# Optimization experiments

Measured on AMD Instinct MI355X. Metric: run time of the kernel, lower is better.

Reference implementation:

```python
import jax, jax.numpy as jnp
import numpy as np

N_BATCHES = 32
N_LABELS = 100


def setup_inputs() -> dict:
    key = jax.random.key(0)
    ks = jax.random.split(key, 7)
    N, D, P = 16384, 2048, 256
    x = jax.random.normal(ks[0], (N, D), dtype=jnp.float32)
    label = jax.random.randint(ks[1], (N,), 0, N_LABELS, dtype=jnp.int64)
    label_batch = jnp.sort(jax.random.randint(ks[2], (N,), 0, N_BATCHES, dtype=jnp.int64))
    W1_w = jax.random.normal(ks[3], (P, D), dtype=jnp.float32) * 0.02
    W1_b = jax.random.normal(ks[4], (P,), dtype=jnp.float32) * 0.02
    W2_w = jax.random.normal(ks[5], (P, D), dtype=jnp.float32) * 0.02
    W2_b = jax.random.normal(ks[6], (P,), dtype=jnp.float32) * 0.02
    return {"x": x, "label": label, "label_batch": label_batch,
            "W1_w": W1_w, "W1_b": W1_b, "W2_w": W2_w, "W2_b": W2_b}


def _loo_diff_label_mean(x, label, label_batch):
    # For each sample i: mean of x over {j : label_batch[j]==label_batch[i] and label[j]!=label[i]}.
    # Rows with no such j are zero (torch code's `continue`). x is detached in the original.
    N = x.shape[0]
    xs = jax.lax.stop_gradient(x)
    seg = label_batch * N_LABELS + label                      # combined (group,label) key
    n_seg = N_BATCHES * N_LABELS
    ones = jnp.ones((N,), dtype=x.dtype)
    sum_bl = jax.ops.segment_sum(xs, seg, num_segments=n_seg)            # [n_seg, D]
    cnt_bl = jax.ops.segment_sum(ones, seg, num_segments=n_seg)          # [n_seg]
    sum_b = jax.ops.segment_sum(xs, label_batch, num_segments=N_BATCHES)  # [NB, D]
    cnt_b = jax.ops.segment_sum(ones, label_batch, num_segments=N_BATCHES)
    diff_sum = sum_b[label_batch] - sum_bl[seg]               # [N, D]
    diff_cnt = cnt_b[label_batch] - cnt_bl[seg]               # [N]
    safe = jnp.maximum(diff_cnt, 1.0)
    mean = diff_sum / safe[:, None]
    return jnp.where((diff_cnt > 0)[:, None], mean, jnp.zeros_like(mean))


def reference(x, label, label_batch, W1_w, W1_b, W2_w, W2_b):
    calc_mean = _loo_diff_label_mean(x, label, label_batch)   # detached aggregate
    return x @ W1_w.T + W1_b + calc_mean @ W2_w.T + W2_b      # W1(x) + W2(mean)
```

## Files before the change

kernel.cpp:

```cpp
#include <hip/hip_runtime.h>
#include <cstdint>

#define N_SAMPLES 16384
#define DIM 2048
#define PDIM 256
#define NB 32
#define NL 100
#define NSEG (NB * NL)

typedef float floatx4 __attribute__((ext_vector_type(4)));
typedef __bf16 bf16x8 __attribute__((ext_vector_type(8)));

__device__ __forceinline__ unsigned short f32_to_bf16(float f) {
    unsigned int u = __float_as_uint(f);
    u += 0x7fffu + ((u >> 16) & 1u);
    return (unsigned short)(u >> 16);
}
__device__ __forceinline__ unsigned int pack_bf16x2(float a, float b) {
    return (unsigned int)f32_to_bf16(a) | ((unsigned int)f32_to_bf16(b) << 16);
}

__global__ __launch_bounds__(256) void prep_kernel(
    const float* __restrict__ W1w, const float* __restrict__ W1b,
    const float* __restrict__ W2w, const float* __restrict__ W2b,
    const int* __restrict__ label, const int* __restrict__ lbatch,
    unsigned short* __restrict__ Wbf, float* __restrict__ bias,
    int* __restrict__ seg, int* __restrict__ cnt, float* __restrict__ SW2)
{
    int i = blockIdx.x * 256 + threadIdx.x;
    Wbf[i]              = f32_to_bf16(W1w[i]);
    Wbf[PDIM * DIM + i] = f32_to_bf16(W2w[i]);
    if (i < PDIM) bias[i] = W1b[i] + W2b[i];
    if (i < N_SAMPLES) seg[i] = lbatch[i] * NL + label[i];
    if (i < NSEG) cnt[i] = 0;
    if (i < NSEG * PDIM / 2) ((float2*)SW2)[i] = make_float2(0.f, 0.f);
}

__global__ __launch_bounds__(256) void hist_kernel(
    const int* __restrict__ seg, int* __restrict__ cnt)
{
    int i = blockIdx.x * 256 + threadIdx.x;
    atomicAdd(&cnt[seg[i]], 1);
}

__global__ __launch_bounds__(256) void xconv_kernel(
    const float* __restrict__ x, unsigned short* __restrict__ xb)
{
    const size_t idx = (size_t)blockIdx.x * 256 + threadIdx.x;
    const float4 a0 = *(const float4*)(x + idx * 8);
    const float4 a1 = *(const float4*)(x + idx * 8 + 4);
    uint4 o;
    o.x = pack_bf16x2(a0.x, a0.y);
    o.y = pack_bf16x2(a0.z, a0.w);
    o.z = pack_bf16x2(a1.x, a1.y);
    o.w = pack_bf16x2(a1.z, a1.w);
    *(uint4*)(xb + idx * 8) = o;
}

__global__ __launch_bounds__(256) void gemm512_kernel(
    const unsigned short* __restrict__ A,
    const unsigned short* __restrict__ Wbf,
    const float* __restrict__ bias, const int* __restrict__ seg,
    float* __restrict__ out, float* __restrict__ SW2)
{
    constexpr int BM = 128, BN = 128, BK = 32;
    __shared__ __align__(16) unsigned short ldsA[BM * BK];
    __shared__ __align__(16) unsigned short ldsB[BN * BK];
    const int tid = threadIdx.x;
    const int lane = tid & 63;
    const int wave = tid >> 6;
    const int wr = wave >> 1, wc = wave & 1;
    const int quad = lane >> 4, l15 = lane & 15;
    const int m0 = blockIdx.x * BM;
    const int n0 = blockIdx.y * BN;
    const int srow = lane >> 2, schunk = lane & 3;

    floatx4 acc[4][4];
    #pragma unroll
    for (int i = 0; i < 4; ++i)
        #pragma unroll
        for (int j = 0; j < 4; ++j) acc[i][j] = (floatx4){0.f, 0.f, 0.f, 0.f};

    const unsigned short* Abase = A + (size_t)(m0 + srow) * DIM + schunk * 8;
    const unsigned short* Bbase = Wbf + (size_t)(n0 + srow) * DIM + schunk * 8;

    for (int kk = 0; kk < DIM; kk += BK) {
        __syncthreads();
        #pragma unroll
        for (int ch = wave; ch < BM / 16; ch += 4)
            __builtin_amdgcn_global_load_lds(
                (const __attribute__((address_space(1))) void*)(Abase + (size_t)ch * 16 * DIM + kk),
                (__attribute__((address_space(3))) void*)&ldsA[ch * 16 * BK], 16, 0, 0);
        #pragma unroll
        for (int ch = wave; ch < BN / 16; ch += 4)
            __builtin_amdgcn_global_load_lds(
                (const __attribute__((address_space(1))) void*)(Bbase + (size_t)ch * 16 * DIM + kk),
                (__attribute__((address_space(3))) void*)&ldsB[ch * 16 * BK], 16, 0, 0);
        __syncthreads();

        bf16x8 af[4], bf[4];
        #pragma unroll
        for (int mi = 0; mi < 4; ++mi)
            af[mi] = *(const bf16x8*)&ldsA[(wr * 64 + mi * 16 + l15) * BK + quad * 8];
        #pragma unroll
        for (int ni = 0; ni < 4; ++ni)
            bf[ni] = *(const bf16x8*)&ldsB[(wc * 64 + ni * 16 + l15) * BK + quad * 8];
        #pragma unroll
        for (int mi = 0; mi < 4; ++mi)
            #pragma unroll
            for (int ni = 0; ni < 4; ++ni)
                acc[mi][ni] = __builtin_amdgcn_mfma_f32_16x16x32_bf16(
                    af[mi], bf[ni], acc[mi][ni], 0, 0, 0);
    }

    if (n0 < PDIM) {
        #pragma unroll
        for (int mi = 0; mi < 4; ++mi) {
            const int rbase = m0 + wr * 64 + mi * 16 + quad * 4;
            #pragma unroll
            for (int ni = 0; ni < 4; ++ni) {
                const int col = n0 + wc * 64 + ni * 16 + l15;
                const float bs = bias[col];
                #pragma unroll
                for (int r = 0; r < 4; ++r)
                    out[(size_t)(rbase + r) * PDIM + col] = acc[mi][ni][r] + bs;
            }
        }
    } else {
        const int c0 = n0 - PDIM;
        #pragma unroll
        for (int mi = 0; mi < 4; ++mi) {
            const int rbase = m0 + wr * 64 + mi * 16 + quad * 4;
            #pragma unroll
            for (int r = 0; r < 4; ++r) {
                const int sr = seg[rbase + r];
                #pragma unroll
                for (int ni = 0; ni < 4; ++ni) {
                    const int col = c0 + wc * 64 + ni * 16 + l15;
                    atomicAdd(&SW2[(size_t)sr * PDIM + col], acc[mi][ni][r]);
                }
            }
        }
    }
}

__global__ __launch_bounds__(256) void finalize_kernel(
    float* __restrict__ SW2, const int* __restrict__ cnt)
{
    const int b = blockIdx.x;
    const int col = threadIdx.x;
    int cb = 0;
    #pragma unroll 4
    for (int l = 0; l < NL; ++l) cb += cnt[b * NL + l];
    float tot = 0.f;
    #pragma unroll 4
    for (int l = 0; l < NL; ++l)
        tot += SW2[(size_t)(b * NL + l) * PDIM + col];
    for (int l = 0; l < NL; ++l) {
        const int s = b * NL + l;
        const int dc = cb - cnt[s];
        const float v = SW2[(size_t)s * PDIM + col];
        SW2[(size_t)s * PDIM + col] = (dc > 0) ? (tot - v) / (float)dc : 0.f;
    }
}

__global__ __launch_bounds__(256) void epilogue_kernel(
    float* __restrict__ out, const float* __restrict__ SW2,
    const int* __restrict__ seg)
{
    const int idx = blockIdx.x * 256 + threadIdx.x;
    const int row = idx >> 6;
    const int c = (idx & 63) * 4;
    float4 v = ((const float4*)out)[idx];
    const float4 s4 = *(const float4*)&SW2[(size_t)seg[row] * PDIM + c];
    v.x += s4.x; v.y += s4.y; v.z += s4.z; v.w += s4.w;
    ((float4*)out)[idx] = v;
}

extern "C" void kernel_launch(void* const* d_in, const int* in_sizes, int n_in,
                              void* d_out, int out_size, void* d_ws, size_t ws_size,
                              hipStream_t stream)
{
    const float* x      = (const float*)d_in[0];
    const int*   label  = (const int*)d_in[1];
    const int*   lbatch = (const int*)d_in[2];
    const float* W1w    = (const float*)d_in[3];
    const float* W1b    = (const float*)d_in[4];
    const float* W2w    = (const float*)d_in[5];
    const float* W2b    = (const float*)d_in[6];
    float* out = (float*)d_out;

    char* ws = (char*)d_ws;
    size_t off = 0;
    auto alloc = [&](size_t bytes) {
        void* p = ws + off;
        off = (off + bytes + 255) & ~(size_t)255;
        return p;
    };
    unsigned short* xb  = (unsigned short*)alloc((size_t)N_SAMPLES * DIM * 2);
    unsigned short* Wbf = (unsigned short*)alloc((size_t)2 * PDIM * DIM * 2);
    float* SW2  = (float*)alloc((size_t)NSEG * PDIM * 4);
    float* bias = (float*)alloc(PDIM * 4);
    int*   seg  = (int*)alloc(N_SAMPLES * 4);
    int*   cnt  = (int*)alloc(NSEG * 4);

    prep_kernel<<<PDIM * DIM / 256, 256, 0, stream>>>(
        W1w, W1b, W2w, W2b, label, lbatch, Wbf, bias, seg, cnt, SW2);

    hist_kernel<<<N_SAMPLES / 256, 256, 0, stream>>>(seg, cnt);

    xconv_kernel<<<(size_t)N_SAMPLES * DIM / 8 / 256, 256, 0, stream>>>(x, xb);

    gemm512_kernel<<<dim3(N_SAMPLES / 128, 4), 256, 0, stream>>>(
        xb, Wbf, bias, seg, out, SW2);

    finalize_kernel<<<NB, 256, 0, stream>>>(SW2, cnt);

    epilogue_kernel<<<(size_t)N_SAMPLES * PDIM / 4 / 256, 256, 0, stream>>>(
        out, SW2, seg);
}
```

Baseline: 305.2 us.

## Split GEMM K dimension in two with atomic accumulation and XCD-aware block mapping

The fused GEMM grid goes from 512 to 1024 blocks by splitting the K dimension into two halves. Partial results are accumulated into the output with atomics, so the output is zeroed in the prep kernel and the bias add moves to the epilogue. Block IDs are remapped so that consecutive blocks on each XCD share M-tiles, which should improve L2 reuse. The aim is better occupancy across the CUs, at the cost of doubled atomic traffic on both the output and the segment sums.

```diff
diff --git a/kernel.cpp b/kernel.cpp
--- a/kernel.cpp
+++ b/kernel.cpp
@@ -25,7 +25,8 @@
     const float* __restrict__ W2w, const float* __restrict__ W2b,
     const int* __restrict__ label, const int* __restrict__ lbatch,
     unsigned short* __restrict__ Wbf, float* __restrict__ bias,
-    int* __restrict__ seg, int* __restrict__ cnt, float* __restrict__ SW2)
+    int* __restrict__ seg, int* __restrict__ cnt, float* __restrict__ SW2,
+    float* __restrict__ out)
 {
     int i = blockIdx.x * 256 + threadIdx.x;
     Wbf[i]              = f32_to_bf16(W1w[i]);
@@ -34,6 +35,9 @@
     if (i < N_SAMPLES) seg[i] = lbatch[i] * NL + label[i];
     if (i < NSEG) cnt[i] = 0;
     if (i < NSEG * PDIM / 2) ((float2*)SW2)[i] = make_float2(0.f, 0.f);
+    const float4 z4 = make_float4(0.f, 0.f, 0.f, 0.f);
+    ((float4*)out)[2 * i]     = z4;
+    ((float4*)out)[2 * i + 1] = z4;
 }
 
 __global__ __launch_bounds__(256) void hist_kernel(
@@ -60,10 +64,10 @@
 __global__ __launch_bounds__(256) void gemm512_kernel(
     const unsigned short* __restrict__ A,
     const unsigned short* __restrict__ Wbf,
-    const float* __restrict__ bias, const int* __restrict__ seg,
+    const int* __restrict__ seg,
     float* __restrict__ out, float* __restrict__ SW2)
 {
-    constexpr int BM = 128, BN = 128, BK = 32;
+    constexpr int BM = 128, BN = 128, BK = 32, KS = 2;
     __shared__ __align__(16) unsigned short ldsA[BM * BK];
     __shared__ __align__(16) unsigned short ldsB[BN * BK];
     const int tid = threadIdx.x;
@@ -71,20 +75,27 @@
     const int wave = tid >> 6;
     const int wr = wave >> 1, wc = wave & 1;
     const int quad = lane >> 4, l15 = lane & 15;
-    const int m0 = blockIdx.x * BM;
-    const int n0 = blockIdx.y * BN;
+
+    const int bid = blockIdx.x;
+    const int j = bid & 7;
+    const int idx = bid >> 3;
+    const int m0 = (j * 16 + (idx & 15)) * BM;
+    const int nz = idx >> 4;
+    const int n0 = (nz & 3) * BN;
+    const int z  = nz >> 2;
+    const int k0 = z * (DIM / KS);
     const int srow = lane >> 2, schunk = lane & 3;
 
     floatx4 acc[4][4];
     #pragma unroll
     for (int i = 0; i < 4; ++i)
         #pragma unroll
-        for (int j = 0; j < 4; ++j) acc[i][j] = (floatx4){0.f, 0.f, 0.f, 0.f};
+        for (int jj = 0; jj < 4; ++jj) acc[i][jj] = (floatx4){0.f, 0.f, 0.f, 0.f};
 
     const unsigned short* Abase = A + (size_t)(m0 + srow) * DIM + schunk * 8;
     const unsigned short* Bbase = Wbf + (size_t)(n0 + srow) * DIM + schunk * 8;
 
-    for (int kk = 0; kk < DIM; kk += BK) {
+    for (int kk = k0; kk < k0 + DIM / KS; kk += BK) {
         __syncthreads();
         #pragma unroll
         for (int ch = wave; ch < BM / 16; ch += 4)
@@ -120,10 +131,9 @@
             #pragma unroll
             for (int ni = 0; ni < 4; ++ni) {
                 const int col = n0 + wc * 64 + ni * 16 + l15;
-                const float bs = bias[col];
                 #pragma unroll
                 for (int r = 0; r < 4; ++r)
-                    out[(size_t)(rbase + r) * PDIM + col] = acc[mi][ni][r] + bs;
+                    atomicAdd(&out[(size_t)(rbase + r) * PDIM + col], acc[mi][ni][r]);
             }
         }
     } else {
@@ -166,14 +176,16 @@
 
 __global__ __launch_bounds__(256) void epilogue_kernel(
     float* __restrict__ out, const float* __restrict__ SW2,
-    const int* __restrict__ seg)
+    const float* __restrict__ bias, const int* __restrict__ seg)
 {
     const int idx = blockIdx.x * 256 + threadIdx.x;
     const int row = idx >> 6;
     const int c = (idx & 63) * 4;
     float4 v = ((const float4*)out)[idx];
+    const float4 b4 = *(const float4*)&bias[c];
     const float4 s4 = *(const float4*)&SW2[(size_t)seg[row] * PDIM + c];
-    v.x += s4.x; v.y += s4.y; v.z += s4.z; v.w += s4.w;
+    v.x += b4.x + s4.x; v.y += b4.y + s4.y;
+    v.z += b4.z + s4.z; v.w += b4.w + s4.w;
     ((float4*)out)[idx] = v;
 }
 
@@ -205,17 +217,16 @@
     int*   cnt  = (int*)alloc(NSEG * 4);
 
     prep_kernel<<<PDIM * DIM / 256, 256, 0, stream>>>(
-        W1w, W1b, W2w, W2b, label, lbatch, Wbf, bias, seg, cnt, SW2);
+        W1w, W1b, W2w, W2b, label, lbatch, Wbf, bias, seg, cnt, SW2, out);
 
     hist_kernel<<<N_SAMPLES / 256, 256, 0, stream>>>(seg, cnt);
 
     xconv_kernel<<<(size_t)N_SAMPLES * DIM / 8 / 256, 256, 0, stream>>>(x, xb);
 
-    gemm512_kernel<<<dim3(N_SAMPLES / 128, 4), 256, 0, stream>>>(
-        xb, Wbf, bias, seg, out, SW2);
+    gemm512_kernel<<<1024, 256, 0, stream>>>(xb, Wbf, seg, out, SW2);
 
     finalize_kernel<<<NB, 256, 0, stream>>>(SW2, cnt);
 
     epilogue_kernel<<<(size_t)N_SAMPLES * PDIM / 4 / 256, 256, 0, stream>>>(
-        out, SW2, seg);
-}
+        out, SW2, bias, seg);
+}
```

New measurement: 343.0 us. +12.4%, slower.

## Fuse fp32-to-bf16 conversion of x into the GEMM's LDS load path

Applied to the files above, without the earlier changes.

Drops the separate x conversion kernel and its bf16 staging buffer. The GEMM now loads fp32 x tiles straight into LDS with an XOR-swizzled layout and converts to bf16 when building the MFMA operands. This removes one full write and read of the converted x. In exchange the GEMM reads twice as many bytes of A per tile (x is read once per N-tile, four times in total), uses more LDS, and does conversion work inside the inner loop.

```diff
diff --git a/kernel.cpp b/kernel.cpp
--- a/kernel.cpp
+++ b/kernel.cpp
@@ -15,9 +15,6 @@
     unsigned int u = __float_as_uint(f);
     u += 0x7fffu + ((u >> 16) & 1u);
     return (unsigned short)(u >> 16);
-}
-__device__ __forceinline__ unsigned int pack_bf16x2(float a, float b) {
-    return (unsigned int)f32_to_bf16(a) | ((unsigned int)f32_to_bf16(b) << 16);
 }
 
 __global__ __launch_bounds__(256) void prep_kernel(
@@ -43,28 +40,14 @@
     atomicAdd(&cnt[seg[i]], 1);
 }
 
-__global__ __launch_bounds__(256) void xconv_kernel(
-    const float* __restrict__ x, unsigned short* __restrict__ xb)
-{
-    const size_t idx = (size_t)blockIdx.x * 256 + threadIdx.x;
-    const float4 a0 = *(const float4*)(x + idx * 8);
-    const float4 a1 = *(const float4*)(x + idx * 8 + 4);
-    uint4 o;
-    o.x = pack_bf16x2(a0.x, a0.y);
-    o.y = pack_bf16x2(a0.z, a0.w);
-    o.z = pack_bf16x2(a1.x, a1.y);
-    o.w = pack_bf16x2(a1.z, a1.w);
-    *(uint4*)(xb + idx * 8) = o;
-}
-
 __global__ __launch_bounds__(256) void gemm512_kernel(
-    const unsigned short* __restrict__ A,
+    const float* __restrict__ x,
     const unsigned short* __restrict__ Wbf,
     const float* __restrict__ bias, const int* __restrict__ seg,
     float* __restrict__ out, float* __restrict__ SW2)
 {
     constexpr int BM = 128, BN = 128, BK = 32;
-    __shared__ __align__(16) unsigned short ldsA[BM * BK];
+    __shared__ __align__(16) float ldsAf[BM * BK];
     __shared__ __align__(16) unsigned short ldsB[BN * BK];
     const int tid = threadIdx.x;
     const int lane = tid & 63;
@@ -73,7 +56,10 @@
     const int quad = lane >> 4, l15 = lane & 15;
     const int m0 = blockIdx.x * BM;
     const int n0 = blockIdx.y * BN;
-    const int srow = lane >> 2, schunk = lane & 3;
+
+    const int arow = lane >> 3;
+    const int achk = (lane & 7) ^ arow;
+    const int brow = lane >> 2, bchk = lane & 3;
 
     floatx4 acc[4][4];
     #pragma unroll
@@ -81,27 +67,34 @@
         #pragma unroll
         for (int j = 0; j < 4; ++j) acc[i][j] = (floatx4){0.f, 0.f, 0.f, 0.f};
 
-    const unsigned short* Abase = A + (size_t)(m0 + srow) * DIM + schunk * 8;
-    const unsigned short* Bbase = Wbf + (size_t)(n0 + srow) * DIM + schunk * 8;
+    const float* Asrc = x + (size_t)(m0 + arow) * DIM + achk * 4;
+    const unsigned short* Bsrc = Wbf + (size_t)(n0 + brow) * DIM + bchk * 8;
 
     for (int kk = 0; kk < DIM; kk += BK) {
         __syncthreads();
         #pragma unroll
-        for (int ch = wave; ch < BM / 16; ch += 4)
+        for (int ch = wave; ch < 16; ch += 4)
             __builtin_amdgcn_global_load_lds(
-                (const __attribute__((address_space(1))) void*)(Abase + (size_t)ch * 16 * DIM + kk),
-                (__attribute__((address_space(3))) void*)&ldsA[ch * 16 * BK], 16, 0, 0);
-        #pragma unroll
-        for (int ch = wave; ch < BN / 16; ch += 4)
+                (const __attribute__((address_space(1))) void*)(Asrc + (size_t)ch * 8 * DIM + kk),
+                (__attribute__((address_space(3))) void*)&ldsAf[ch * 256], 16, 0, 0);
+        #pragma unroll
+        for (int ch = wave; ch < 8; ch += 4)
             __builtin_amdgcn_global_load_lds(
-                (const __attribute__((address_space(1))) void*)(Bbase + (size_t)ch * 16 * DIM + kk),
-                (__attribute__((address_space(3))) void*)&ldsB[ch * 16 * BK], 16, 0, 0);
+                (const __attribute__((address_space(1))) void*)(Bsrc + (size_t)ch * 16 * DIM + kk),
+                (__attribute__((address_space(3))) void*)&ldsB[ch * 512], 16, 0, 0);
         __syncthreads();
 
         bf16x8 af[4], bf[4];
         #pragma unroll
-        for (int mi = 0; mi < 4; ++mi)
-            af[mi] = *(const bf16x8*)&ldsA[(wr * 64 + mi * 16 + l15) * BK + quad * 8];
+        for (int mi = 0; mi < 4; ++mi) {
+            const int ar = wr * 64 + mi * 16 + l15;
+            const int s = ar & 7;
+            const float* pa = &ldsAf[ar * BK];
+            floatx4 lo = *(const floatx4*)(pa + (((quad * 2)     ^ s) << 2));
+            floatx4 hi = *(const floatx4*)(pa + (((quad * 2 + 1) ^ s) << 2));
+            af[mi] = (bf16x8){ (__bf16)lo[0], (__bf16)lo[1], (__bf16)lo[2], (__bf16)lo[3],
+                               (__bf16)hi[0], (__bf16)hi[1], (__bf16)hi[2], (__bf16)hi[3] };
+        }
         #pragma unroll
         for (int ni = 0; ni < 4; ++ni)
             bf[ni] = *(const bf16x8*)&ldsB[(wc * 64 + ni * 16 + l15) * BK + quad * 8];
@@ -197,7 +190,6 @@
         off = (off + bytes + 255) & ~(size_t)255;
         return p;
     };
-    unsigned short* xb  = (unsigned short*)alloc((size_t)N_SAMPLES * DIM * 2);
     unsigned short* Wbf = (unsigned short*)alloc((size_t)2 * PDIM * DIM * 2);
     float* SW2  = (float*)alloc((size_t)NSEG * PDIM * 4);
     float* bias = (float*)alloc(PDIM * 4);
@@ -209,10 +201,8 @@
 
     hist_kernel<<<N_SAMPLES / 256, 256, 0, stream>>>(seg, cnt);
 
-    xconv_kernel<<<(size_t)N_SAMPLES * DIM / 8 / 256, 256, 0, stream>>>(x, xb);
-
     gemm512_kernel<<<dim3(N_SAMPLES / 128, 4), 256, 0, stream>>>(
-        xb, Wbf, bias, seg, out, SW2);
+        x, Wbf, bias, seg, out, SW2);
 
     finalize_kernel<<<NB, 256, 0, stream>>>(SW2, cnt);
 
```

After: 286.9 us. 1.06x faster.
